# Performance work log

Measured on AMD Instinct MI355X. Metric: run time of the kernel, lower is better.

## Reference

```python
import jax, jax.numpy as jnp
import numpy as np

N = 50000      # nodes
E = 800000     # edges (avg degree 16)
D_IN, D_H, D_OUT = 128, 256, 128


def setup_inputs() -> dict:
    key = jax.random.key(0)
    ks = jax.random.split(key, 8)
    x = jax.random.normal(ks[0], (N, D_IN), dtype=jnp.float32)
    edge_index = jax.random.randint(ks[1], (2, E), 0, N, dtype=jnp.int64)
    s1 = 1.0 / np.sqrt(D_IN).astype(np.float32)
    s2 = 1.0 / np.sqrt(D_H).astype(np.float32)
    return {
        "x": x,
        "edge_index": edge_index,
        "W1l": jax.random.normal(ks[2], (D_H, D_IN), jnp.float32) * s1,
        "b1l": jnp.zeros((D_H,), jnp.float32),
        "W1r": jax.random.normal(ks[3], (D_H, D_IN), jnp.float32) * s1,
        "W2l": jax.random.normal(ks[4], (D_OUT, D_H), jnp.float32) * s2,
        "b2l": jnp.zeros((D_OUT,), jnp.float32),
        "W2r": jax.random.normal(ks[5], (D_OUT, D_H), jnp.float32) * s2,
    }


def sage_conv(x, src, dst, Wl, bl, Wr):
    # mean-aggregate source features into destination nodes
    agg = jax.ops.segment_sum(x[src], dst, num_segments=N)           # [N, d_in]
    deg = jax.ops.segment_sum(jnp.ones((src.shape[0],), x.dtype), dst, num_segments=N)
    mean = agg / jnp.maximum(deg, 1.0)[:, None]
    # lin_l(mean_agg) + lin_r(x_root); lin_r has no bias (PyG SAGEConv default)
    return mean @ Wl.T + bl + x @ Wr.T


def reference(x, edge_index, W1l, b1l, W1r, W2l, b2l, W2r):
    src, dst = edge_index[0], edge_index[1]
    h = sage_conv(x, src, dst, W1l, b1l, W1r)
    h = jax.nn.relu(h)  # dropout inactive in eval mode
    return sage_conv(h, src, dst, W2l, b2l, W2r)
```

## Files before the change

### kernel.cpp

```cpp
#include <hip/hip_runtime.h>


typedef __attribute__((ext_vector_type(8))) short bf16x8;
typedef __attribute__((ext_vector_type(4))) float floatx4;

__device__ inline unsigned short f2b(float f) {
  unsigned int x = __float_as_uint(f);
  unsigned int r = (x + 0x7fffu + ((x >> 16) & 1u)) >> 16;
  return (unsigned short)r;
}

__global__ void wpack_kernel(const float* __restrict__ W1l, const float* __restrict__ W1r,
                             const float* __restrict__ W2l, const float* __restrict__ W2r,
                             unsigned short* __restrict__ Wc1, unsigned short* __restrict__ Wc2) {
  int i = blockIdx.x * blockDim.x + threadIdx.x;
  int j = i >> 8, k = i & 255;
  float v1 = (k < 128) ? W1l[j * 128 + k] : W1r[j * 128 + (k - 128)];
  Wc1[i] = f2b(v1);
  float v2 = (j < 128) ? W2l[j * 256 + k] : W2r[(j - 128) * 256 + k];
  Wc2[i] = f2b(v2);
}

__global__ void xcvt_kernel(const float* __restrict__ x, unsigned short* __restrict__ A1, int N) {
  int i = blockIdx.x * blockDim.x + threadIdx.x;
  if (i >= N * 32) return;
  int n = i >> 5, c = (i & 31) * 4;
  float4 v = *(const float4*)(x + (size_t)n * 128 + c);
  uint2 p;
  p.x = (unsigned int)f2b(v.x) | ((unsigned int)f2b(v.y) << 16);
  p.y = (unsigned int)f2b(v.z) | ((unsigned int)f2b(v.w) << 16);
  *(uint2*)(A1 + (size_t)n * 256 + 128 + c) = p;
}

__global__ void zero_int_kernel(int* __restrict__ p, int n) {
  int i = blockIdx.x * blockDim.x + threadIdx.x;
  if (i < n) p[i] = 0;
}

__global__ void hist_kernel(const int* __restrict__ dst, int* __restrict__ cnt, int E) {
  int e = blockIdx.x * blockDim.x + threadIdx.x;
  if (e < E) atomicAdd(&cnt[dst[e]], 1);
}

__global__ __launch_bounds__(1024) void scan_blocks_kernel(const int* __restrict__ cnt,
                                                           int* __restrict__ off,
                                                           int* __restrict__ bsum, int N) {
  __shared__ int wsum[16];
  __shared__ int wincl[16];
  const int tid = threadIdx.x;
  const int lane = tid & 63;
  const int wv = tid >> 6;
  const int i = blockIdx.x * 1024 + tid;
  const int v = (i < N) ? cnt[i] : 0;
  int s = v;
#pragma unroll
  for (int o = 1; o < 64; o <<= 1) {
    int t = __shfl_up(s, o, 64);
    if (lane >= o) s += t;
  }
  if (lane == 63) wsum[wv] = s;
  __syncthreads();
  if (tid < 16) {
    int ws = wsum[tid];
#pragma unroll
    for (int o = 1; o < 16; o <<= 1) {
      int t = __shfl_up(ws, o, 16);
      if ((tid & 15) >= o) ws += t;
    }
    wincl[tid] = ws;
  }
  __syncthreads();
  const int wo = wv ? wincl[wv - 1] : 0;
  if (i < N) off[i] = wo + s - v;
  if (tid == 1023) bsum[blockIdx.x] = wo + s;
}

__global__ void scan_sums_kernel(int* __restrict__ bsum, int* __restrict__ off, int B, int N, int E) {
  int lane = threadIdx.x;
  int v = (lane < B) ? bsum[lane] : 0;
  int s = v;
#pragma unroll
  for (int o = 1; o < 64; o <<= 1) {
    int t = __shfl_up(s, o, 64);
    if (lane >= o) s += t;
  }
  if (lane < B) bsum[lane] = s - v;
  if (lane == 0) off[N] = E;
}

__global__ __launch_bounds__(1024) void scan_add_kernel(int* __restrict__ off, int* __restrict__ cur,
                                                        const int* __restrict__ bsum, int N) {
  int i = blockIdx.x * 1024 + threadIdx.x;
  if (i < N) {
    int o = off[i] + bsum[blockIdx.x];
    off[i] = o;
    cur[i] = o;
  }
}

__global__ void fill_kernel(const int* __restrict__ src, const int* __restrict__ dst,
                            int* __restrict__ cur, int* __restrict__ csr, int E) {
  int e = blockIdx.x * blockDim.x + threadIdx.x;
  if (e < E) {
    int p = atomicAdd(&cur[dst[e]], 1);
    csr[p] = src[e];
  }
}

__global__ void gather1_kernel(const unsigned short* __restrict__ feat,
                               const int* __restrict__ csr, const int* __restrict__ off,
                               unsigned short* __restrict__ ob, int N) {
  int tid = blockIdx.x * blockDim.x + threadIdx.x;
  int g = tid >> 5;
  if (g >= N) return;
  int lane = tid & 31;
  const int s0 = off[g], s1 = off[g + 1];
  float a0 = 0, a1 = 0, a2 = 0, a3 = 0, c0 = 0, c1 = 0, c2 = 0, c3 = 0;
  int e = s0;
  for (; e + 1 < s1; e += 2) {
    int i0 = csr[e], i1 = csr[e + 1];
    uint2 u = *(const uint2*)(feat + (size_t)i0 * 256 + lane * 4);
    uint2 w = *(const uint2*)(feat + (size_t)i1 * 256 + lane * 4);
    a0 += __uint_as_float(u.x << 16); a1 += __uint_as_float(u.x & 0xffff0000u);
    a2 += __uint_as_float(u.y << 16); a3 += __uint_as_float(u.y & 0xffff0000u);
    c0 += __uint_as_float(w.x << 16); c1 += __uint_as_float(w.x & 0xffff0000u);
    c2 += __uint_as_float(w.y << 16); c3 += __uint_as_float(w.y & 0xffff0000u);
  }
  if (e < s1) {
    int i0 = csr[e];
    uint2 u = *(const uint2*)(feat + (size_t)i0 * 256 + lane * 4);
    a0 += __uint_as_float(u.x << 16); a1 += __uint_as_float(u.x & 0xffff0000u);
    a2 += __uint_as_float(u.y << 16); a3 += __uint_as_float(u.y & 0xffff0000u);
  }
  const float inv = 1.0f / fmaxf((float)(s1 - s0), 1.0f);
  a0 = (a0 + c0) * inv; a1 = (a1 + c1) * inv; a2 = (a2 + c2) * inv; a3 = (a3 + c3) * inv;
  uint2 p;
  p.x = (unsigned int)f2b(a0) | ((unsigned int)f2b(a1) << 16);
  p.y = (unsigned int)f2b(a2) | ((unsigned int)f2b(a3) << 16);
  *(uint2*)(ob + (size_t)g * 256 + lane * 4) = p;
}

__global__ void gather2_kernel(const unsigned short* __restrict__ t,
                               const int* __restrict__ csr, const int* __restrict__ off,
                               float* __restrict__ out, int N) {
  int tid = blockIdx.x * blockDim.x + threadIdx.x;
  int g = tid >> 5;
  if (g >= N) return;
  int lane = tid & 31;
  const int s0 = off[g], s1 = off[g + 1];
  float a0 = 0, a1 = 0, a2 = 0, a3 = 0, c0 = 0, c1 = 0, c2 = 0, c3 = 0;
  int e = s0;
  for (; e + 1 < s1; e += 2) {
    int i0 = csr[e], i1 = csr[e + 1];
    uint2 u = *(const uint2*)(t + (size_t)i0 * 128 + lane * 4);
    uint2 w = *(const uint2*)(t + (size_t)i1 * 128 + lane * 4);
    a0 += __uint_as_float(u.x << 16); a1 += __uint_as_float(u.x & 0xffff0000u);
    a2 += __uint_as_float(u.y << 16); a3 += __uint_as_float(u.y & 0xffff0000u);
    c0 += __uint_as_float(w.x << 16); c1 += __uint_as_float(w.x & 0xffff0000u);
    c2 += __uint_as_float(w.y << 16); c3 += __uint_as_float(w.y & 0xffff0000u);
  }
  if (e < s1) {
    int i0 = csr[e];
    uint2 u = *(const uint2*)(t + (size_t)i0 * 128 + lane * 4);
    a0 += __uint_as_float(u.x << 16); a1 += __uint_as_float(u.x & 0xffff0000u);
    a2 += __uint_as_float(u.y << 16); a3 += __uint_as_float(u.y & 0xffff0000u);
  }
  const float inv = 1.0f / fmaxf((float)(s1 - s0), 1.0f);
  float4* o = (float4*)(out + (size_t)g * 128) + lane;
  float4 c = *o;
  c.x += (a0 + c0) * inv; c.y += (a1 + c1) * inv;
  c.z += (a2 + c2) * inv; c.w += (a3 + c3) * inv;
  *o = c;
}

template <int MODE>
__global__ __launch_bounds__(256, 2)
void gemm_bf16(const unsigned short* __restrict__ A, const unsigned short* __restrict__ W,
               const float* __restrict__ bias, unsigned short* __restrict__ Hout,
               float* __restrict__ Fout, int M) {
  constexpr int LDA = 72;
  __shared__ __align__(16) unsigned short As[128 * LDA];
  __shared__ __align__(16) unsigned short Ws[128 * LDA];
  const int t = threadIdx.x;
  const int lane = t & 63;
  const int wave = t >> 6;
  const int wm = (wave & 1) * 64;
  const int wn = (wave >> 1) * 64;
  const int l15 = lane & 15;
  const int quad = lane >> 4;
  const int m_blk = blockIdx.x * 128;
  const int j_blk = blockIdx.y * 128;

  floatx4 acc[4][4] = {};

  for (int kc = 0; kc < 256; kc += 64) {
    __syncthreads();
#pragma unroll
    for (int i = 0; i < 4; i++) {
      int c = t + 256 * i;
      int row = c >> 3;
      int col = (c & 7) * 8;
      int ar = m_blk + row;
      if (ar >= M) ar = M - 1;
      uint4 av = *(const uint4*)(A + (size_t)ar * 256 + kc + col);
      *(uint4*)(As + row * LDA + col) = av;
      uint4 wv = *(const uint4*)(W + (size_t)(j_blk + row) * 256 + kc + col);
      *(uint4*)(Ws + row * LDA + col) = wv;
    }
    __syncthreads();
#pragma unroll
    for (int ks = 0; ks < 64; ks += 32) {
      bf16x8 af[4], bfr[4];
#pragma unroll
      for (int mt = 0; mt < 4; mt++)
        af[mt] = *(const bf16x8*)(As + (wm + mt * 16 + l15) * LDA + ks + quad * 8);
#pragma unroll
      for (int nt = 0; nt < 4; nt++)
        bfr[nt] = *(const bf16x8*)(Ws + (wn + nt * 16 + l15) * LDA + ks + quad * 8);
#pragma unroll
      for (int mt = 0; mt < 4; mt++)
#pragma unroll
        for (int nt = 0; nt < 4; nt++)
          acc[mt][nt] = __builtin_amdgcn_mfma_f32_16x16x32_bf16(af[mt], bfr[nt], acc[mt][nt], 0, 0, 0);
    }
  }

#pragma unroll
  for (int mt = 0; mt < 4; mt++) {
#pragma unroll
    for (int nt = 0; nt < 4; nt++) {
      const int jl = wn + nt * 16 + l15;
      float bv = 0.f;
      if (MODE == 0) bv = bias[j_blk + jl];
      else if (j_blk != 0) bv = bias[jl];
#pragma unroll
      for (int r = 0; r < 4; r++) {
        const int node = m_blk + wm + mt * 16 + quad * 4 + r;
        if (node >= M) continue;
        const float v = acc[mt][nt][r];
        if (MODE == 0) {
          Hout[(size_t)node * 256 + j_blk + jl] = f2b(fmaxf(v + bv, 0.f));
        } else if (j_blk == 0) {
          Hout[(size_t)node * 128 + jl] = f2b(v);
        } else {
          Fout[(size_t)node * 128 + jl] = v + bv;
        }
      }
    }
  }
}

extern "C" void kernel_launch(void* const* d_in, const int* in_sizes, int n_in,
                              void* d_out, int out_size, void* d_ws, size_t ws_size,
                              hipStream_t stream) {
  const float* x   = (const float*)d_in[0];
  const int*  eidx = (const int*)d_in[1];
  const float* W1l = (const float*)d_in[2];
  const float* b1l = (const float*)d_in[3];
  const float* W1r = (const float*)d_in[4];
  const float* W2l = (const float*)d_in[5];
  const float* b2l = (const float*)d_in[6];
  const float* W2r = (const float*)d_in[7];
  float* out = (float*)d_out;

  const int N = in_sizes[0] / 128;
  const int E = in_sizes[1] / 2;
  const int* src = eidx;
  const int* dst = eidx + E;

  int* cnt  = (int*)d_ws;
  int* off  = cnt + N;
  int* bsum = off + N + 1;
  int* csr  = bsum + 64;
  size_t ioff = ((size_t)(N + N + 1 + 64 + E) * 4 + 15) & ~(size_t)15;
  unsigned short* A1  = (unsigned short*)((char*)d_ws + ioff);
  unsigned short* h   = A1 + (size_t)N * 256;
  unsigned short* tb  = h + (size_t)N * 256;
  unsigned short* Wc1 = tb + (size_t)N * 128;
  unsigned short* Wc2 = Wc1 + 65536;

  const int SB = (N + 1023) / 1024;

  wpack_kernel<<<256, 256, 0, stream>>>(W1l, W1r, W2l, W2r, Wc1, Wc2);
  xcvt_kernel<<<(N * 32 + 255) / 256, 256, 0, stream>>>(x, A1, N);

  zero_int_kernel<<<(N + 255) / 256, 256, 0, stream>>>(cnt, N);
  hist_kernel<<<(E + 255) / 256, 256, 0, stream>>>(dst, cnt, E);
  scan_blocks_kernel<<<SB, 1024, 0, stream>>>(cnt, off, bsum, N);
  scan_sums_kernel<<<1, 64, 0, stream>>>(bsum, off, SB, N, E);
  scan_add_kernel<<<SB, 1024, 0, stream>>>(off, cnt, bsum, N);
  fill_kernel<<<(E + 255) / 256, 256, 0, stream>>>(src, dst, cnt, csr, E);

  const int gblocks = (int)(((size_t)N * 32 + 255) / 256);
  gather1_kernel<<<gblocks, 256, 0, stream>>>(A1 + 128, csr, off, A1, N);

  dim3 gg((N + 127) / 128, 2);
  gemm_bf16<0><<<gg, 256, 0, stream>>>(A1, Wc1, b1l, h, nullptr, N);
  gemm_bf16<1><<<gg, 256, 0, stream>>>(h, Wc2, b2l, tb, out, N);
  gather2_kernel<<<gblocks, 256, 0, stream>>>(tb, csr, off, out, N);
}
```

Baseline: 316.4 us.

## Fuse prep kernels, merge scan passes, bucket CSR fill, widen gather loads

Measured after the change: 301.0 us. -4.9%, faster.

```diff
diff --git a/kernel.cpp b/kernel.cpp
--- a/kernel.cpp
+++ b/kernel.cpp
@@ -9,32 +9,33 @@
   unsigned int r = (x + 0x7fffu + ((x >> 16) & 1u)) >> 16;
   return (unsigned short)r;
 }
-
-__global__ void wpack_kernel(const float* __restrict__ W1l, const float* __restrict__ W1r,
-                             const float* __restrict__ W2l, const float* __restrict__ W2r,
-                             unsigned short* __restrict__ Wc1, unsigned short* __restrict__ Wc2) {
+__device__ inline float blo(unsigned int u) { return __uint_as_float(u << 16); }
+__device__ inline float bhi(unsigned int u) { return __uint_as_float(u & 0xffff0000u); }
+
+__global__ void prep_kernel(const float* __restrict__ x,
+                            const float* __restrict__ W1l, const float* __restrict__ W1r,
+                            const float* __restrict__ W2l, const float* __restrict__ W2r,
+                            unsigned short* __restrict__ Wc1, unsigned short* __restrict__ Wc2,
+                            unsigned short* __restrict__ A1,
+                            int* __restrict__ cnt, int* __restrict__ off, int N, int E) {
   int i = blockIdx.x * blockDim.x + threadIdx.x;
-  int j = i >> 8, k = i & 255;
-  float v1 = (k < 128) ? W1l[j * 128 + k] : W1r[j * 128 + (k - 128)];
-  Wc1[i] = f2b(v1);
-  float v2 = (j < 128) ? W2l[j * 256 + k] : W2r[(j - 128) * 256 + k];
-  Wc2[i] = f2b(v2);
-}
-
-__global__ void xcvt_kernel(const float* __restrict__ x, unsigned short* __restrict__ A1, int N) {
-  int i = blockIdx.x * blockDim.x + threadIdx.x;
-  if (i >= N * 32) return;
-  int n = i >> 5, c = (i & 31) * 4;
-  float4 v = *(const float4*)(x + (size_t)n * 128 + c);
-  uint2 p;
-  p.x = (unsigned int)f2b(v.x) | ((unsigned int)f2b(v.y) << 16);
-  p.y = (unsigned int)f2b(v.z) | ((unsigned int)f2b(v.w) << 16);
-  *(uint2*)(A1 + (size_t)n * 256 + 128 + c) = p;
-}
-
-__global__ void zero_int_kernel(int* __restrict__ p, int n) {
-  int i = blockIdx.x * blockDim.x + threadIdx.x;
-  if (i < n) p[i] = 0;
+  if (i < 65536) {
+    int j = i >> 8, k = i & 255;
+    float v1 = (k < 128) ? W1l[j * 128 + k] : W1r[j * 128 + (k - 128)];
+    Wc1[i] = f2b(v1);
+    float v2 = (j < 128) ? W2l[j * 256 + k] : W2r[(j - 128) * 256 + k];
+    Wc2[i] = f2b(v2);
+  }
+  if (i < N) cnt[i] = 0;
+  if (i == 0) off[N] = E;
+  if (i < N * 32) {
+    int n = i >> 5, c = (i & 31) * 4;
+    float4 v = *(const float4*)(x + (size_t)n * 128 + c);
+    uint2 p;
+    p.x = (unsigned int)f2b(v.x) | ((unsigned int)f2b(v.y) << 16);
+    p.y = (unsigned int)f2b(v.z) | ((unsigned int)f2b(v.w) << 16);
+    *(uint2*)(A1 + (size_t)n * 256 + 128 + c) = p;
+  }
 }
 
 __global__ void hist_kernel(const int* __restrict__ dst, int* __restrict__ cnt, int E) {
@@ -75,102 +76,122 @@
   if (tid == 1023) bsum[blockIdx.x] = wo + s;
 }
 
-__global__ void scan_sums_kernel(int* __restrict__ bsum, int* __restrict__ off, int B, int N, int E) {
-  int lane = threadIdx.x;
-  int v = (lane < B) ? bsum[lane] : 0;
-  int s = v;
-#pragma unroll
-  for (int o = 1; o < 64; o <<= 1) {
-    int t = __shfl_up(s, o, 64);
-    if (lane >= o) s += t;
-  }
-  if (lane < B) bsum[lane] = s - v;
-  if (lane == 0) off[N] = E;
-}
-
 __global__ __launch_bounds__(1024) void scan_add_kernel(int* __restrict__ off, int* __restrict__ cur,
-                                                        const int* __restrict__ bsum, int N) {
-  int i = blockIdx.x * 1024 + threadIdx.x;
+                                                        const int* __restrict__ bsum, int N, int SB) {
+  __shared__ int bofs[64];
+  const int tid = threadIdx.x;
+  if (tid < 64) {
+    int v = (tid < SB) ? bsum[tid] : 0;
+    int s = v;
+#pragma unroll
+    for (int o = 1; o < 64; o <<= 1) {
+      int t = __shfl_up(s, o, 64);
+      if (tid >= o) s += t;
+    }
+    bofs[tid] = s - v;
+  }
+  __syncthreads();
+  int i = blockIdx.x * 1024 + tid;
   if (i < N) {
-    int o = off[i] + bsum[blockIdx.x];
+    int o = off[i] + bofs[blockIdx.x];
     off[i] = o;
     cur[i] = o;
   }
 }
 
 __global__ void fill_kernel(const int* __restrict__ src, const int* __restrict__ dst,
-                            int* __restrict__ cur, int* __restrict__ csr, int E) {
-  int e = blockIdx.x * blockDim.x + threadIdx.x;
-  if (e < E) {
-    int p = atomicAdd(&cur[dst[e]], 1);
-    csr[p] = src[e];
-  }
+                            int* __restrict__ cur, int* __restrict__ csr, int E, int chunks) {
+  int pass = blockIdx.x / chunks;
+  int c = blockIdx.x - pass * chunks;
+  int e = c * 256 + threadIdx.x;
+  if (e >= E) return;
+  int d = dst[e];
+  if ((d >> 14) != pass) return;
+  int p = atomicAdd(&cur[d], 1);
+  csr[p] = src[e];
 }
 
 __global__ void gather1_kernel(const unsigned short* __restrict__ feat,
                                const int* __restrict__ csr, const int* __restrict__ off,
                                unsigned short* __restrict__ ob, int N) {
-  int tid = blockIdx.x * blockDim.x + threadIdx.x;
-  int g = tid >> 5;
-  if (g >= N) return;
-  int lane = tid & 31;
-  const int s0 = off[g], s1 = off[g + 1];
-  float a0 = 0, a1 = 0, a2 = 0, a3 = 0, c0 = 0, c1 = 0, c2 = 0, c3 = 0;
-  int e = s0;
-  for (; e + 1 < s1; e += 2) {
-    int i0 = csr[e], i1 = csr[e + 1];
-    uint2 u = *(const uint2*)(feat + (size_t)i0 * 256 + lane * 4);
-    uint2 w = *(const uint2*)(feat + (size_t)i1 * 256 + lane * 4);
-    a0 += __uint_as_float(u.x << 16); a1 += __uint_as_float(u.x & 0xffff0000u);
-    a2 += __uint_as_float(u.y << 16); a3 += __uint_as_float(u.y & 0xffff0000u);
-    c0 += __uint_as_float(w.x << 16); c1 += __uint_as_float(w.x & 0xffff0000u);
-    c2 += __uint_as_float(w.y << 16); c3 += __uint_as_float(w.y & 0xffff0000u);
+  int wid = (blockIdx.x * blockDim.x + threadIdx.x) >> 6;
+  if (wid >= N) return;
+  const int lane = threadIdx.x & 63;
+  const int sub = lane >> 4;
+  const int col8 = (lane & 15) * 8;
+  const int s0 = off[wid], s1 = off[wid + 1];
+  float a[8] = {};
+  int e = s0 + sub;
+  for (; e + 4 < s1; e += 8) {
+    int i0 = csr[e], i1 = csr[e + 4];
+    uint4 u = *(const uint4*)(feat + (size_t)i0 * 256 + col8);
+    uint4 w = *(const uint4*)(feat + (size_t)i1 * 256 + col8);
+    a[0] += blo(u.x); a[1] += bhi(u.x); a[2] += blo(u.y); a[3] += bhi(u.y);
+    a[4] += blo(u.z); a[5] += bhi(u.z); a[6] += blo(u.w); a[7] += bhi(u.w);
+    a[0] += blo(w.x); a[1] += bhi(w.x); a[2] += blo(w.y); a[3] += bhi(w.y);
+    a[4] += blo(w.z); a[5] += bhi(w.z); a[6] += blo(w.w); a[7] += bhi(w.w);
   }
   if (e < s1) {
     int i0 = csr[e];
-    uint2 u = *(const uint2*)(feat + (size_t)i0 * 256 + lane * 4);
-    a0 += __uint_as_float(u.x << 16); a1 += __uint_as_float(u.x & 0xffff0000u);
-    a2 += __uint_as_float(u.y << 16); a3 += __uint_as_float(u.y & 0xffff0000u);
-  }
-  const float inv = 1.0f / fmaxf((float)(s1 - s0), 1.0f);
-  a0 = (a0 + c0) * inv; a1 = (a1 + c1) * inv; a2 = (a2 + c2) * inv; a3 = (a3 + c3) * inv;
-  uint2 p;
-  p.x = (unsigned int)f2b(a0) | ((unsigned int)f2b(a1) << 16);
-  p.y = (unsigned int)f2b(a2) | ((unsigned int)f2b(a3) << 16);
-  *(uint2*)(ob + (size_t)g * 256 + lane * 4) = p;
+    uint4 u = *(const uint4*)(feat + (size_t)i0 * 256 + col8);
+    a[0] += blo(u.x); a[1] += bhi(u.x); a[2] += blo(u.y); a[3] += bhi(u.y);
+    a[4] += blo(u.z); a[5] += bhi(u.z); a[6] += blo(u.w); a[7] += bhi(u.w);
+  }
+#pragma unroll
+  for (int k = 0; k < 8; k++) {
+    a[k] += __shfl_xor(a[k], 16, 64);
+    a[k] += __shfl_xor(a[k], 32, 64);
+  }
+  if (sub == 0) {
+    const float inv = 1.0f / fmaxf((float)(s1 - s0), 1.0f);
+    uint4 p;
+    p.x = (unsigned int)f2b(a[0] * inv) | ((unsigned int)f2b(a[1] * inv) << 16);
+    p.y = (unsigned int)f2b(a[2] * inv) | ((unsigned int)f2b(a[3] * inv) << 16);
+    p.z = (unsigned int)f2b(a[4] * inv) | ((unsigned int)f2b(a[5] * inv) << 16);
+    p.w = (unsigned int)f2b(a[6] * inv) | ((unsigned int)f2b(a[7] * inv) << 16);
+    *(uint4*)(ob + (size_t)wid * 256 + col8) = p;
+  }
 }
 
 __global__ void gather2_kernel(const unsigned short* __restrict__ t,
                                const int* __restrict__ csr, const int* __restrict__ off,
                                float* __restrict__ out, int N) {
-  int tid = blockIdx.x * blockDim.x + threadIdx.x;
-  int g = tid >> 5;
-  if (g >= N) return;
-  int lane = tid & 31;
-  const int s0 = off[g], s1 = off[g + 1];
-  float a0 = 0, a1 = 0, a2 = 0, a3 = 0, c0 = 0, c1 = 0, c2 = 0, c3 = 0;
-  int e = s0;
-  for (; e + 1 < s1; e += 2) {
-    int i0 = csr[e], i1 = csr[e + 1];
-    uint2 u = *(const uint2*)(t + (size_t)i0 * 128 + lane * 4);
-    uint2 w = *(const uint2*)(t + (size_t)i1 * 128 + lane * 4);
-    a0 += __uint_as_float(u.x << 16); a1 += __uint_as_float(u.x & 0xffff0000u);
-    a2 += __uint_as_float(u.y << 16); a3 += __uint_as_float(u.y & 0xffff0000u);
-    c0 += __uint_as_float(w.x << 16); c1 += __uint_as_float(w.x & 0xffff0000u);
-    c2 += __uint_as_float(w.y << 16); c3 += __uint_as_float(w.y & 0xffff0000u);
+  int wid = (blockIdx.x * blockDim.x + threadIdx.x) >> 6;
+  if (wid >= N) return;
+  const int lane = threadIdx.x & 63;
+  const int sub = lane >> 4;
+  const int col8 = (lane & 15) * 8;
+  const int s0 = off[wid], s1 = off[wid + 1];
+  float a[8] = {};
+  int e = s0 + sub;
+  for (; e + 4 < s1; e += 8) {
+    int i0 = csr[e], i1 = csr[e + 4];
+    uint4 u = *(const uint4*)(t + (size_t)i0 * 128 + col8);
+    uint4 w = *(const uint4*)(t + (size_t)i1 * 128 + col8);
+    a[0] += blo(u.x); a[1] += bhi(u.x); a[2] += blo(u.y); a[3] += bhi(u.y);
+    a[4] += blo(u.z); a[5] += bhi(u.z); a[6] += blo(u.w); a[7] += bhi(u.w);
+    a[0] += blo(w.x); a[1] += bhi(w.x); a[2] += blo(w.y); a[3] += bhi(w.y);
+    a[4] += blo(w.z); a[5] += bhi(w.z); a[6] += blo(w.w); a[7] += bhi(w.w);
   }
   if (e < s1) {
     int i0 = csr[e];
-    uint2 u = *(const uint2*)(t + (size_t)i0 * 128 + lane * 4);
-    a0 += __uint_as_float(u.x << 16); a1 += __uint_as_float(u.x & 0xffff0000u);
-    a2 += __uint_as_float(u.y << 16); a3 += __uint_as_float(u.y & 0xffff0000u);
-  }
-  const float inv = 1.0f / fmaxf((float)(s1 - s0), 1.0f);
-  float4* o = (float4*)(out + (size_t)g * 128) + lane;
-  float4 c = *o;
-  c.x += (a0 + c0) * inv; c.y += (a1 + c1) * inv;
-  c.z += (a2 + c2) * inv; c.w += (a3 + c3) * inv;
-  *o = c;
+    uint4 u = *(const uint4*)(t + (size_t)i0 * 128 + col8);
+    a[0] += blo(u.x); a[1] += bhi(u.x); a[2] += blo(u.y); a[3] += bhi(u.y);
+    a[4] += blo(u.z); a[5] += bhi(u.z); a[6] += blo(u.w); a[7] += bhi(u.w);
+  }
+#pragma unroll
+  for (int k = 0; k < 8; k++) {
+    a[k] += __shfl_xor(a[k], 16, 64);
+    a[k] += __shfl_xor(a[k], 32, 64);
+  }
+  if (sub == 0) {
+    const float inv = 1.0f / fmaxf((float)(s1 - s0), 1.0f);
+    float4* o = (float4*)(out + (size_t)wid * 128 + col8);
+    float4 c0 = o[0], c1 = o[1];
+    c0.x += a[0] * inv; c0.y += a[1] * inv; c0.z += a[2] * inv; c0.w += a[3] * inv;
+    c1.x += a[4] * inv; c1.y += a[5] * inv; c1.z += a[6] * inv; c1.w += a[7] * inv;
+    o[0] = c0; o[1] = c1;
+  }
 }
 
 template <int MODE>
@@ -281,17 +302,16 @@
 
   const int SB = (N + 1023) / 1024;
 
-  wpack_kernel<<<256, 256, 0, stream>>>(W1l, W1r, W2l, W2r, Wc1, Wc2);
-  xcvt_kernel<<<(N * 32 + 255) / 256, 256, 0, stream>>>(x, A1, N);
-
-  zero_int_kernel<<<(N + 255) / 256, 256, 0, stream>>>(cnt, N);
+  prep_kernel<<<(N * 32 + 255) / 256, 256, 0, stream>>>(x, W1l, W1r, W2l, W2r,
+                                                        Wc1, Wc2, A1, cnt, off, N, E);
   hist_kernel<<<(E + 255) / 256, 256, 0, stream>>>(dst, cnt, E);
   scan_blocks_kernel<<<SB, 1024, 0, stream>>>(cnt, off, bsum, N);
-  scan_sums_kernel<<<1, 64, 0, stream>>>(bsum, off, SB, N, E);
-  scan_add_kernel<<<SB, 1024, 0, stream>>>(off, cnt, bsum, N);
-  fill_kernel<<<(E + 255) / 256, 256, 0, stream>>>(src, dst, cnt, csr, E);
-
-  const int gblocks = (int)(((size_t)N * 32 + 255) / 256);
+  scan_add_kernel<<<SB, 1024, 0, stream>>>(off, cnt, bsum, N, SB);
+
+  const int chunks = (E + 255) / 256;
+  fill_kernel<<<chunks * 4, 256, 0, stream>>>(src, dst, cnt, csr, E, chunks);
+
+  const int gblocks = (N + 3) / 4;
   gather1_kernel<<<gblocks, 256, 0, stream>>>(A1 + 128, csr, off, A1, N);
 
   dim3 gg((N + 127) / 128, 2);
```
